# Optimization experiments

Measured on AMD Instinct MI355X. Metric: run time of the kernel, lower is better.

The kernel has to match this reference:

```python
import jax, jax.numpy as jnp
import numpy as np

B, D, E, T, P = 65536, 256, 256, 128, 8  # batch, memory_dim, edge_feat_dim, time_dim, num_prototypes
LN_EPS = 1e-6
NORM_EPS = 1e-6


def _layer_norm(x, w, b):
    mu = jnp.mean(x, axis=-1, keepdims=True)
    var = jnp.mean(jnp.square(x - mu), axis=-1, keepdims=True)
    return (x - mu) / jnp.sqrt(var + LN_EPS) * w + b


def setup_inputs() -> dict:
    key = jax.random.key(0)
    ks = jax.random.split(key, 10)
    qin = D + E + T            # query_proj in_features
    gin = 2 * D + T            # gate_proj in_features
    return {
        "raw_memory": jax.random.normal(ks[0], (B, D), dtype=jnp.float32),
        "node_features": jax.random.normal(ks[1], (B, D), dtype=jnp.float32),
        "edge_features": jax.random.normal(ks[2], (B, E), dtype=jnp.float32),
        "time_encoding": jax.random.normal(ks[3], (B, T), dtype=jnp.float32),
        "prototypes": jax.random.normal(ks[4], (B, P, D), dtype=jnp.float32),
        # learned params (xavier gain=0.1 -> small)
        "Wq": jax.random.normal(ks[5], (D, qin), dtype=jnp.float32) * (0.1 * np.sqrt(2.0 / (D + qin))),
        "bq": jnp.zeros((D,), dtype=jnp.float32),
        "Wg": jax.random.normal(ks[6], (1, gin), dtype=jnp.float32) * (0.1 * np.sqrt(2.0 / (1 + gin))),
        "bg": jnp.zeros((1,), dtype=jnp.float32),
        "temperature": jnp.ones((1,), dtype=jnp.float32),
        "ln_w": jnp.ones((D,), dtype=jnp.float32),
        "ln_b": jnp.zeros((D,), dtype=jnp.float32),
    }


def reference(raw_memory, node_features, edge_features, time_encoding, prototypes,
              Wq, bq, Wg, bg, temperature, ln_w, ln_b):
    # query projection (inputs are finite so _sanitize_tensor is identity)
    q_in = jnp.concatenate([raw_memory, edge_features, time_encoding], axis=-1)  # [B, D+E+T]
    query = jnp.tanh(_layer_norm(q_in @ Wq.T + bq, ln_w, ln_b))                   # [B, D]

    # cosine similarity to per-node prototypes (F.normalize uses max(norm, eps))
    qn = query / jnp.maximum(jnp.linalg.norm(query, axis=-1, keepdims=True), NORM_EPS)
    pn = prototypes / jnp.maximum(jnp.linalg.norm(prototypes, axis=-1, keepdims=True), NORM_EPS)
    sim = jnp.clip(jnp.einsum('bd,bpd->bp', qn, pn), -10.0, 10.0)                 # [B, P]
    temp = jnp.clip(temperature, 0.5, 5.0)
    sim = sim / (temp + 0.01)

    attn = jnp.clip(jax.nn.softmax(sim, axis=-1), 0.0, 1.0)                       # [B, P]
    candidate = jnp.clip(jnp.einsum('bp,bpd->bd', attn, prototypes), -5.0, 5.0)   # [B, D]

    # gated update
    g_in = jnp.clip(jnp.concatenate([raw_memory, candidate, time_encoding], axis=-1), -50.0, 50.0)
    gate = jax.nn.sigmoid(jnp.clip(g_in @ Wg.T + bg, -10.0, 10.0))                # [B, 1]
    updated = (1.0 - gate) * raw_memory + gate * candidate
    updated = jnp.clip(_layer_norm(updated, ln_w, ln_b), -10.0, 10.0)
    return updated
```

## Files before the change

kernel.cpp:

```cpp
#include <hip/hip_runtime.h>
#include <cstdint>
#include <cstddef>

#define D 256
#define E 256
#define T 128
#define QIN 640
#define P 8
#define R 16
#define KP 648
#define DP 260

typedef __attribute__((ext_vector_type(8))) short bf16x8;
typedef __attribute__((ext_vector_type(4))) float f32x4;

__device__ __forceinline__ ushort f2bf(float f) {
  uint32_t u = __float_as_uint(f);
  u += 0x7fffu + ((u >> 16) & 1u);
  return (ushort)(u >> 16);
}

__device__ __forceinline__ float wsum(float v) {
#pragma unroll
  for (int o = 32; o > 0; o >>= 1) v += __shfl_xor(v, o, 64);
  return v;
}

__device__ __forceinline__ void wsum2(float& a, float& b) {
#pragma unroll
  for (int o = 32; o > 0; o >>= 1) {
    a += __shfl_xor(a, o, 64);
    b += __shfl_xor(b, o, 64);
  }
}

__device__ __forceinline__ float clampf(float x, float lo, float hi) {
  return fminf(fmaxf(x, lo), hi);
}

__global__ void prep_w2_kernel(const float* __restrict__ Wq, ushort* __restrict__ W2) {
  const int idx = blockIdx.x * 256 + threadIdx.x;
  const int n = idx / QIN;
  const int k = idx - n * QIN;
  W2[((((k >> 3) * D + n) << 3)) + (k & 7)] = f2bf(Wq[idx]);
}

template <bool PRE>
__global__ __launch_bounds__(256, 4) void fused_kernel(
    const float* __restrict__ raw, const float* __restrict__ edge,
    const float* __restrict__ tim, const float* __restrict__ proto,
    const float* __restrict__ Wq, const ushort* __restrict__ W2,
    const float* __restrict__ bq, const float* __restrict__ Wg,
    const float* __restrict__ bg, const float* __restrict__ temp,
    const float* __restrict__ lnw, const float* __restrict__ lnb,
    float* __restrict__ out) {
  __shared__ ushort qa[R][KP];
  __shared__ float qpre[R][DP];

  const int tid = threadIdx.x;
  const int r0 = blockIdx.x * R;

#pragma unroll
  for (int it = 0; it < (R * QIN / 4) / 256; ++it) {
    const int flat = it * 256 + tid;
    const int r = flat / (QIN / 4);
    const int p4 = (flat - r * (QIN / 4)) * 4;
    const size_t g = (size_t)(r0 + r);
    float4 v;
    if (p4 < D)          v = *(const float4*)(raw + g * D + p4);
    else if (p4 < D + E) v = *(const float4*)(edge + g * E + (p4 - D));
    else                 v = *(const float4*)(tim + g * T + (p4 - D - E));
    ushort4 h;
    h.x = f2bf(v.x); h.y = f2bf(v.y); h.z = f2bf(v.z); h.w = f2bf(v.w);
    *(ushort4*)&qa[r][p4] = h;
  }
  __syncthreads();

  const int w = tid >> 6;
  const int lane = tid & 63;
  const int lr = lane & 15;
  const int lh = lane >> 4;

  {
    f32x4 acc[4];
#pragma unroll
    for (int c = 0; c < 4; ++c) acc[c] = (f32x4){0.f, 0.f, 0.f, 0.f};

    for (int kb = 0; kb < QIN; kb += 32) {
      const bf16x8 af = *(const bf16x8*)&qa[lr][kb + lh * 8];
#pragma unroll
      for (int c = 0; c < 4; ++c) {
        const int n = w * 64 + c * 16 + lr;
        bf16x8 bfv;
        if (PRE) {
          bfv = *(const bf16x8*)&W2[(((kb >> 3) + lh) * D + n) << 3];
        } else {
          const float* src = Wq + (size_t)n * QIN + kb + lh * 8;
          const float4 a0 = *(const float4*)src;
          const float4 a1 = *(const float4*)(src + 4);
          bfv[0] = (short)f2bf(a0.x); bfv[1] = (short)f2bf(a0.y);
          bfv[2] = (short)f2bf(a0.z); bfv[3] = (short)f2bf(a0.w);
          bfv[4] = (short)f2bf(a1.x); bfv[5] = (short)f2bf(a1.y);
          bfv[6] = (short)f2bf(a1.z); bfv[7] = (short)f2bf(a1.w);
        }
        acc[c] = __builtin_amdgcn_mfma_f32_16x16x32_bf16(af, bfv, acc[c], 0, 0, 0);
      }
    }

#pragma unroll
    for (int c = 0; c < 4; ++c) {
      const int n = w * 64 + c * 16 + lr;
      const float bqv = bq[n];
#pragma unroll
      for (int i = 0; i < 4; ++i) qpre[lh * 4 + i][n] = acc[c][i] + bqv;
    }
  }
  __syncthreads();

  const float4 lnw4 = *(const float4*)(lnw + 4 * lane);
  const float4 lnb4 = *(const float4*)(lnb + 4 * lane);
  const float lw[4] = {lnw4.x, lnw4.y, lnw4.z, lnw4.w};
  const float lb[4] = {lnb4.x, lnb4.y, lnb4.z, lnb4.w};
  const float4 wga = *(const float4*)(Wg + 4 * lane);
  const float4 wgb = *(const float4*)(Wg + D + 4 * lane);
  const float2 wgt = *(const float2*)(Wg + 2 * D + 2 * lane);
  const float bgv = bg[0];
  const float invt = 1.0f / (clampf(temp[0], 0.5f, 5.0f) + 0.01f);

  for (int r = w; r < R; r += 4) {
    const size_t g = (size_t)(r0 + r);

    const float4 x4 = *(const float4*)&qpre[r][4 * lane];
    float x[4] = {x4.x, x4.y, x4.z, x4.w};
    float s = x[0] + x[1] + x[2] + x[3];
    const float mu = wsum(s) * (1.0f / 256.0f);
    float dx[4];
    float v = 0.f;
#pragma unroll
    for (int i = 0; i < 4; ++i) { dx[i] = x[i] - mu; v += dx[i] * dx[i]; }
    const float rstd = 1.0f / sqrtf(wsum(v) * (1.0f / 256.0f) + 1e-6f);
    float q[4];
    float qs = 0.f;
#pragma unroll
    for (int i = 0; i < 4; ++i) {
      q[i] = tanhf(dx[i] * rstd * lw[i] + lb[i]);
      qs += q[i] * q[i];
    }
    const float qdiv = fmaxf(sqrtf(wsum(qs)), 1e-6f);

    const float* pb = proto + (g * P) * D + 4 * lane;
    float pv[P][4];
    float sim[P];
#pragma unroll
    for (int p = 0; p < P; ++p) {
      const float4 p4 = *(const float4*)(pb + (size_t)p * D);
      pv[p][0] = p4.x; pv[p][1] = p4.y; pv[p][2] = p4.z; pv[p][3] = p4.w;
      float dt = q[0] * p4.x + q[1] * p4.y + q[2] * p4.z + q[3] * p4.w;
      float pn = p4.x * p4.x + p4.y * p4.y + p4.z * p4.z + p4.w * p4.w;
      wsum2(dt, pn);
      const float pdiv = fmaxf(sqrtf(pn), 1e-6f);
      sim[p] = clampf(dt / (qdiv * pdiv), -10.0f, 10.0f) * invt;
    }

    float m = sim[0];
#pragma unroll
    for (int p = 1; p < P; ++p) m = fmaxf(m, sim[p]);
    float es[P];
    float ssum = 0.f;
#pragma unroll
    for (int p = 0; p < P; ++p) { es[p] = expf(sim[p] - m); ssum += es[p]; }
    const float sinv = 1.0f / ssum;
    float cand[4] = {0.f, 0.f, 0.f, 0.f};
#pragma unroll
    for (int p = 0; p < P; ++p) {
      const float a = clampf(es[p] * sinv, 0.0f, 1.0f);
#pragma unroll
      for (int i = 0; i < 4; ++i) cand[i] = fmaf(a, pv[p][i], cand[i]);
    }
#pragma unroll
    for (int i = 0; i < 4; ++i) cand[i] = clampf(cand[i], -5.0f, 5.0f);

    const float4 raw4 = *(const float4*)(raw + g * D + 4 * lane);
    const float rr[4] = {raw4.x, raw4.y, raw4.z, raw4.w};
    const float2 t2 = *(const float2*)(tim + g * T + 2 * lane);
    float gsum =
        clampf(rr[0], -50.f, 50.f) * wga.x + clampf(rr[1], -50.f, 50.f) * wga.y +
        clampf(rr[2], -50.f, 50.f) * wga.z + clampf(rr[3], -50.f, 50.f) * wga.w +
        clampf(cand[0], -50.f, 50.f) * wgb.x + clampf(cand[1], -50.f, 50.f) * wgb.y +
        clampf(cand[2], -50.f, 50.f) * wgb.z + clampf(cand[3], -50.f, 50.f) * wgb.w +
        clampf(t2.x, -50.f, 50.f) * wgt.x + clampf(t2.y, -50.f, 50.f) * wgt.y;
    const float z = clampf(wsum(gsum) + bgv, -10.0f, 10.0f);
    const float gate = 1.0f / (1.0f + expf(-z));

    float upd[4];
    float s2 = 0.f;
#pragma unroll
    for (int i = 0; i < 4; ++i) {
      upd[i] = (1.0f - gate) * rr[i] + gate * cand[i];
      s2 += upd[i];
    }
    const float mu2 = wsum(s2) * (1.0f / 256.0f);
    float du[4];
    float v2 = 0.f;
#pragma unroll
    for (int i = 0; i < 4; ++i) { du[i] = upd[i] - mu2; v2 += du[i] * du[i]; }
    const float rstd2 = 1.0f / sqrtf(wsum(v2) * (1.0f / 256.0f) + 1e-6f);
    float4 y;
    y.x = clampf(du[0] * rstd2 * lw[0] + lb[0], -10.0f, 10.0f);
    y.y = clampf(du[1] * rstd2 * lw[1] + lb[1], -10.0f, 10.0f);
    y.z = clampf(du[2] * rstd2 * lw[2] + lb[2], -10.0f, 10.0f);
    y.w = clampf(du[3] * rstd2 * lw[3] + lb[3], -10.0f, 10.0f);
    *(float4*)(out + g * D + 4 * lane) = y;
  }
}

extern "C" void kernel_launch(void* const* d_in, const int* in_sizes, int n_in,
                              void* d_out, int out_size, void* d_ws, size_t ws_size,
                              hipStream_t stream) {
  const float* raw   = (const float*)d_in[0];
  const float* edge  = (const float*)d_in[2];
  const float* tim   = (const float*)d_in[3];
  const float* proto = (const float*)d_in[4];
  const float* Wq    = (const float*)d_in[5];
  const float* bq    = (const float*)d_in[6];
  const float* Wg    = (const float*)d_in[7];
  const float* bg    = (const float*)d_in[8];
  const float* temp  = (const float*)d_in[9];
  const float* lnw   = (const float*)d_in[10];
  const float* lnb   = (const float*)d_in[11];
  float* out = (float*)d_out;

  const int B = in_sizes[0] / D;
  const int nblk = B / R;

  const bool pre = ws_size >= (size_t)(QIN * D * sizeof(ushort));
  if (pre) {
    ushort* W2 = (ushort*)d_ws;
    prep_w2_kernel<<<(QIN * D) / 256, 256, 0, stream>>>(Wq, W2);
    fused_kernel<true><<<nblk, 256, 0, stream>>>(raw, edge, tim, proto, Wq, W2,
                                                 bq, Wg, bg, temp, lnw, lnb, out);
  } else {
    fused_kernel<false><<<nblk, 256, 0, stream>>>(raw, edge, tim, proto, Wq,
                                                  (const ushort*)nullptr, bq, Wg,
                                                  bg, temp, lnw, lnb, out);
  }
}
```

Before: 227.1 us.

## Prefetch prototype rows into registers before GEMM and double-buffer across rows

Issues the first row's prototype loads for each wave before the MFMA projection loop, so their latency hides behind the GEMM. The per-row epilogue is unrolled into four calls that software-pipeline the next row's prototype loads (and hoist raw/time loads) while the current row is computed. This adds about 64 extra live VGPRs per thread under a launch bound of 4 blocks per CU, which risks spills or lower occupancy.

```diff
diff --git a/kernel.cpp b/kernel.cpp
--- a/kernel.cpp
+++ b/kernel.cpp
@@ -80,6 +80,13 @@
   const int lane = tid & 63;
   const int lr = lane & 15;
   const int lh = lane >> 4;
+
+  float4 bufA[P], bufB[P];
+  {
+    const float* pb0 = proto + ((size_t)(r0 + w) * P) * D + 4 * lane;
+#pragma unroll
+    for (int p = 0; p < P; ++p) bufA[p] = *(const float4*)(pb0 + (size_t)p * D);
+  }
 
   {
     f32x4 acc[4];
@@ -127,8 +134,16 @@
   const float bgv = bg[0];
   const float invt = 1.0f / (clampf(temp[0], 0.5f, 5.0f) + 0.01f);
 
-  for (int r = w; r < R; r += 4) {
+  auto process = [&](int r, float4* cur, float4* nxt, bool pre) {
     const size_t g = (size_t)(r0 + r);
+
+    if (pre) {
+      const float* pbn = proto + ((g + 4) * P) * D + 4 * lane;
+#pragma unroll
+      for (int p = 0; p < P; ++p) nxt[p] = *(const float4*)(pbn + (size_t)p * D);
+    }
+    const float4 raw4 = *(const float4*)(raw + g * D + 4 * lane);
+    const float2 t2 = *(const float2*)(tim + g * T + 2 * lane);
 
     const float4 x4 = *(const float4*)&qpre[r][4 * lane];
     float x[4] = {x4.x, x4.y, x4.z, x4.w};
@@ -148,13 +163,10 @@
     }
     const float qdiv = fmaxf(sqrtf(wsum(qs)), 1e-6f);
 
-    const float* pb = proto + (g * P) * D + 4 * lane;
-    float pv[P][4];
     float sim[P];
 #pragma unroll
     for (int p = 0; p < P; ++p) {
-      const float4 p4 = *(const float4*)(pb + (size_t)p * D);
-      pv[p][0] = p4.x; pv[p][1] = p4.y; pv[p][2] = p4.z; pv[p][3] = p4.w;
+      const float4 p4 = cur[p];
       float dt = q[0] * p4.x + q[1] * p4.y + q[2] * p4.z + q[3] * p4.w;
       float pn = p4.x * p4.x + p4.y * p4.y + p4.z * p4.z + p4.w * p4.w;
       wsum2(dt, pn);
@@ -165,24 +177,23 @@
     float m = sim[0];
 #pragma unroll
     for (int p = 1; p < P; ++p) m = fmaxf(m, sim[p]);
-    float es[P];
     float ssum = 0.f;
 #pragma unroll
-    for (int p = 0; p < P; ++p) { es[p] = expf(sim[p] - m); ssum += es[p]; }
+    for (int p = 0; p < P; ++p) { sim[p] = expf(sim[p] - m); ssum += sim[p]; }
     const float sinv = 1.0f / ssum;
     float cand[4] = {0.f, 0.f, 0.f, 0.f};
 #pragma unroll
     for (int p = 0; p < P; ++p) {
-      const float a = clampf(es[p] * sinv, 0.0f, 1.0f);
-#pragma unroll
-      for (int i = 0; i < 4; ++i) cand[i] = fmaf(a, pv[p][i], cand[i]);
+      const float a = clampf(sim[p] * sinv, 0.0f, 1.0f);
+      cand[0] = fmaf(a, cur[p].x, cand[0]);
+      cand[1] = fmaf(a, cur[p].y, cand[1]);
+      cand[2] = fmaf(a, cur[p].z, cand[2]);
+      cand[3] = fmaf(a, cur[p].w, cand[3]);
     }
 #pragma unroll
     for (int i = 0; i < 4; ++i) cand[i] = clampf(cand[i], -5.0f, 5.0f);
 
-    const float4 raw4 = *(const float4*)(raw + g * D + 4 * lane);
     const float rr[4] = {raw4.x, raw4.y, raw4.z, raw4.w};
-    const float2 t2 = *(const float2*)(tim + g * T + 2 * lane);
     float gsum =
         clampf(rr[0], -50.f, 50.f) * wga.x + clampf(rr[1], -50.f, 50.f) * wga.y +
         clampf(rr[2], -50.f, 50.f) * wga.z + clampf(rr[3], -50.f, 50.f) * wga.w +
@@ -211,7 +222,12 @@
     y.z = clampf(du[2] * rstd2 * lw[2] + lb[2], -10.0f, 10.0f);
     y.w = clampf(du[3] * rstd2 * lw[3] + lb[3], -10.0f, 10.0f);
     *(float4*)(out + g * D + 4 * lane) = y;
-  }
+  };
+
+  process(w,      bufA, bufB, true);
+  process(w + 4,  bufB, bufA, true);
+  process(w + 8,  bufA, bufB, true);
+  process(w + 12, bufB, bufA, false);
 }
 
 extern "C" void kernel_launch(void* const* d_in, const int* in_sizes, int n_in,
```

Result: faster. 220.2 us (-3.0%).

## Split fused kernel into query-projection and prototype-streaming kernels via bf16 workspace

Applied to the files above, without the earlier changes.

Splits the fused kernel into two. One does the GEMM, layer norm and tanh, writing a normalized bf16 query to workspace. The other is a lightweight one-row-per-wave kernel that streams the prototypes and computes the attention, gate and final layer norm. This decouples the bandwidth-heavy prototype reads from the MFMA/LDS phase so the streaming kernel can run at higher occupancy. The cost is extra global traffic for the qn round trip and re-reading raw and time, plus one more launch and bf16 rounding of the normalized query.

```diff
diff --git a/kernel.cpp b/kernel.cpp
--- a/kernel.cpp
+++ b/kernel.cpp
@@ -19,6 +19,9 @@
   u += 0x7fffu + ((u >> 16) & 1u);
   return (ushort)(u >> 16);
 }
+__device__ __forceinline__ float bf2f(ushort h) {
+  return __uint_as_float(((uint32_t)h) << 16);
+}
 
 __device__ __forceinline__ float wsum(float v) {
 #pragma unroll
@@ -45,15 +48,11 @@
   W2[((((k >> 3) * D + n) << 3)) + (k & 7)] = f2bf(Wq[idx]);
 }
 
-template <bool PRE>
-__global__ __launch_bounds__(256, 4) void fused_kernel(
+__global__ __launch_bounds__(256, 4) void qn_kernel(
     const float* __restrict__ raw, const float* __restrict__ edge,
-    const float* __restrict__ tim, const float* __restrict__ proto,
-    const float* __restrict__ Wq, const ushort* __restrict__ W2,
-    const float* __restrict__ bq, const float* __restrict__ Wg,
-    const float* __restrict__ bg, const float* __restrict__ temp,
-    const float* __restrict__ lnw, const float* __restrict__ lnb,
-    float* __restrict__ out) {
+    const float* __restrict__ tim, const ushort* __restrict__ W2,
+    const float* __restrict__ bq, const float* __restrict__ lnw,
+    const float* __restrict__ lnb, ushort* __restrict__ qn) {
   __shared__ ushort qa[R][KP];
   __shared__ float qpre[R][DP];
 
@@ -91,22 +90,194 @@
 #pragma unroll
       for (int c = 0; c < 4; ++c) {
         const int n = w * 64 + c * 16 + lr;
-        bf16x8 bfv;
-        if (PRE) {
-          bfv = *(const bf16x8*)&W2[(((kb >> 3) + lh) * D + n) << 3];
-        } else {
-          const float* src = Wq + (size_t)n * QIN + kb + lh * 8;
-          const float4 a0 = *(const float4*)src;
-          const float4 a1 = *(const float4*)(src + 4);
-          bfv[0] = (short)f2bf(a0.x); bfv[1] = (short)f2bf(a0.y);
-          bfv[2] = (short)f2bf(a0.z); bfv[3] = (short)f2bf(a0.w);
-          bfv[4] = (short)f2bf(a1.x); bfv[5] = (short)f2bf(a1.y);
-          bfv[6] = (short)f2bf(a1.z); bfv[7] = (short)f2bf(a1.w);
-        }
+        const bf16x8 bfv = *(const bf16x8*)&W2[(((kb >> 3) + lh) * D + n) << 3];
         acc[c] = __builtin_amdgcn_mfma_f32_16x16x32_bf16(af, bfv, acc[c], 0, 0, 0);
       }
     }
-
+#pragma unroll
+    for (int c = 0; c < 4; ++c) {
+      const int n = w * 64 + c * 16 + lr;
+      const float bqv = bq[n];
+#pragma unroll
+      for (int i = 0; i < 4; ++i) qpre[lh * 4 + i][n] = acc[c][i] + bqv;
+    }
+  }
+  __syncthreads();
+
+  const float4 lnw4 = *(const float4*)(lnw + 4 * lane);
+  const float4 lnb4 = *(const float4*)(lnb + 4 * lane);
+  const float lw[4] = {lnw4.x, lnw4.y, lnw4.z, lnw4.w};
+  const float lb[4] = {lnb4.x, lnb4.y, lnb4.z, lnb4.w};
+
+  for (int r = w; r < R; r += 4) {
+    const size_t g = (size_t)(r0 + r);
+    const float4 x4 = *(const float4*)&qpre[r][4 * lane];
+    float x[4] = {x4.x, x4.y, x4.z, x4.w};
+    const float mu = wsum(x[0] + x[1] + x[2] + x[3]) * (1.0f / 256.0f);
+    float dx[4];
+    float v = 0.f;
+#pragma unroll
+    for (int i = 0; i < 4; ++i) { dx[i] = x[i] - mu; v += dx[i] * dx[i]; }
+    const float rstd = 1.0f / sqrtf(wsum(v) * (1.0f / 256.0f) + 1e-6f);
+    float q[4];
+    float qs = 0.f;
+#pragma unroll
+    for (int i = 0; i < 4; ++i) {
+      q[i] = tanhf(dx[i] * rstd * lw[i] + lb[i]);
+      qs += q[i] * q[i];
+    }
+    const float qinv = 1.0f / fmaxf(sqrtf(wsum(qs)), 1e-6f);
+    ushort4 h;
+    h.x = f2bf(q[0] * qinv); h.y = f2bf(q[1] * qinv);
+    h.z = f2bf(q[2] * qinv); h.w = f2bf(q[3] * qinv);
+    *(ushort4*)(qn + g * D + 4 * lane) = h;
+  }
+}
+
+__global__ __launch_bounds__(256, 5) void stream_kernel(
+    const float* __restrict__ raw, const float* __restrict__ tim,
+    const float* __restrict__ proto, const ushort* __restrict__ qn,
+    const float* __restrict__ Wg, const float* __restrict__ bg,
+    const float* __restrict__ temp, const float* __restrict__ lnw,
+    const float* __restrict__ lnb, float* __restrict__ out) {
+  const int tid = threadIdx.x;
+  const int w = tid >> 6;
+  const int lane = tid & 63;
+  const size_t g = (size_t)blockIdx.x * 4 + w;
+
+  const float* pb = proto + (g * P) * D + 4 * lane;
+  float4 pv[P];
+#pragma unroll
+  for (int p = 0; p < P; ++p) pv[p] = *(const float4*)(pb + (size_t)p * D);
+  const ushort4 qh = *(const ushort4*)(qn + g * D + 4 * lane);
+  const float4 raw4 = *(const float4*)(raw + g * D + 4 * lane);
+  const float2 t2 = *(const float2*)(tim + g * T + 2 * lane);
+
+  const float4 lnw4 = *(const float4*)(lnw + 4 * lane);
+  const float4 lnb4 = *(const float4*)(lnb + 4 * lane);
+  const float4 wga = *(const float4*)(Wg + 4 * lane);
+  const float4 wgb = *(const float4*)(Wg + D + 4 * lane);
+  const float2 wgt = *(const float2*)(Wg + 2 * D + 2 * lane);
+  const float bgv = bg[0];
+  const float invt = 1.0f / (clampf(temp[0], 0.5f, 5.0f) + 0.01f);
+
+  const float q[4] = {bf2f(qh.x), bf2f(qh.y), bf2f(qh.z), bf2f(qh.w)};
+
+  float sim[P];
+#pragma unroll
+  for (int p = 0; p < P; ++p) {
+    const float4 p4 = pv[p];
+    float dt = q[0] * p4.x + q[1] * p4.y + q[2] * p4.z + q[3] * p4.w;
+    float pn = p4.x * p4.x + p4.y * p4.y + p4.z * p4.z + p4.w * p4.w;
+    wsum2(dt, pn);
+    const float pdiv = fmaxf(sqrtf(pn), 1e-6f);
+    sim[p] = clampf(dt / pdiv, -10.0f, 10.0f) * invt;
+  }
+
+  float m = sim[0];
+#pragma unroll
+  for (int p = 1; p < P; ++p) m = fmaxf(m, sim[p]);
+  float ssum = 0.f;
+#pragma unroll
+  for (int p = 0; p < P; ++p) { sim[p] = expf(sim[p] - m); ssum += sim[p]; }
+  const float sinv = 1.0f / ssum;
+  float cand[4] = {0.f, 0.f, 0.f, 0.f};
+#pragma unroll
+  for (int p = 0; p < P; ++p) {
+    const float a = clampf(sim[p] * sinv, 0.0f, 1.0f);
+    cand[0] = fmaf(a, pv[p].x, cand[0]);
+    cand[1] = fmaf(a, pv[p].y, cand[1]);
+    cand[2] = fmaf(a, pv[p].z, cand[2]);
+    cand[3] = fmaf(a, pv[p].w, cand[3]);
+  }
+#pragma unroll
+  for (int i = 0; i < 4; ++i) cand[i] = clampf(cand[i], -5.0f, 5.0f);
+
+  const float rr[4] = {raw4.x, raw4.y, raw4.z, raw4.w};
+  float gsum =
+      clampf(rr[0], -50.f, 50.f) * wga.x + clampf(rr[1], -50.f, 50.f) * wga.y +
+      clampf(rr[2], -50.f, 50.f) * wga.z + clampf(rr[3], -50.f, 50.f) * wga.w +
+      clampf(cand[0], -50.f, 50.f) * wgb.x + clampf(cand[1], -50.f, 50.f) * wgb.y +
+      clampf(cand[2], -50.f, 50.f) * wgb.z + clampf(cand[3], -50.f, 50.f) * wgb.w +
+      clampf(t2.x, -50.f, 50.f) * wgt.x + clampf(t2.y, -50.f, 50.f) * wgt.y;
+  const float z = clampf(wsum(gsum) + bgv, -10.0f, 10.0f);
+  const float gate = 1.0f / (1.0f + expf(-z));
+
+  float upd[4];
+  float s2 = 0.f;
+#pragma unroll
+  for (int i = 0; i < 4; ++i) {
+    upd[i] = (1.0f - gate) * rr[i] + gate * cand[i];
+    s2 += upd[i];
+  }
+  const float mu2 = wsum(s2) * (1.0f / 256.0f);
+  float du[4];
+  float v2 = 0.f;
+#pragma unroll
+  for (int i = 0; i < 4; ++i) { du[i] = upd[i] - mu2; v2 += du[i] * du[i]; }
+  const float rstd2 = 1.0f / sqrtf(wsum(v2) * (1.0f / 256.0f) + 1e-6f);
+  float4 y;
+  y.x = clampf(du[0] * rstd2 * lnw4.x + lnb4.x, -10.0f, 10.0f);
+  y.y = clampf(du[1] * rstd2 * lnw4.y + lnb4.y, -10.0f, 10.0f);
+  y.z = clampf(du[2] * rstd2 * lnw4.z + lnb4.z, -10.0f, 10.0f);
+  y.w = clampf(du[3] * rstd2 * lnw4.w + lnb4.w, -10.0f, 10.0f);
+  *(float4*)(out + g * D + 4 * lane) = y;
+}
+
+__global__ __launch_bounds__(256, 4) void fused_kernel(
+    const float* __restrict__ raw, const float* __restrict__ edge,
+    const float* __restrict__ tim, const float* __restrict__ proto,
+    const float* __restrict__ Wq, const float* __restrict__ bq,
+    const float* __restrict__ Wg, const float* __restrict__ bg,
+    const float* __restrict__ temp, const float* __restrict__ lnw,
+    const float* __restrict__ lnb, float* __restrict__ out) {
+  __shared__ ushort qa[R][KP];
+  __shared__ float qpre[R][DP];
+
+  const int tid = threadIdx.x;
+  const int r0 = blockIdx.x * R;
+
+#pragma unroll
+  for (int it = 0; it < (R * QIN / 4) / 256; ++it) {
+    const int flat = it * 256 + tid;
+    const int r = flat / (QIN / 4);
+    const int p4 = (flat - r * (QIN / 4)) * 4;
+    const size_t g = (size_t)(r0 + r);
+    float4 v;
+    if (p4 < D)          v = *(const float4*)(raw + g * D + p4);
+    else if (p4 < D + E) v = *(const float4*)(edge + g * E + (p4 - D));
+    else                 v = *(const float4*)(tim + g * T + (p4 - D - E));
+    ushort4 h;
+    h.x = f2bf(v.x); h.y = f2bf(v.y); h.z = f2bf(v.z); h.w = f2bf(v.w);
+    *(ushort4*)&qa[r][p4] = h;
+  }
+  __syncthreads();
+
+  const int w = tid >> 6;
+  const int lane = tid & 63;
+  const int lr = lane & 15;
+  const int lh = lane >> 4;
+
+  {
+    f32x4 acc[4];
+#pragma unroll
+    for (int c = 0; c < 4; ++c) acc[c] = (f32x4){0.f, 0.f, 0.f, 0.f};
+    for (int kb = 0; kb < QIN; kb += 32) {
+      const bf16x8 af = *(const bf16x8*)&qa[lr][kb + lh * 8];
+#pragma unroll
+      for (int c = 0; c < 4; ++c) {
+        const int n = w * 64 + c * 16 + lr;
+        const float* src = Wq + (size_t)n * QIN + kb + lh * 8;
+        const float4 a0 = *(const float4*)src;
+        const float4 a1 = *(const float4*)(src + 4);
+        bf16x8 bfv;
+        bfv[0] = (short)f2bf(a0.x); bfv[1] = (short)f2bf(a0.y);
+        bfv[2] = (short)f2bf(a0.z); bfv[3] = (short)f2bf(a0.w);
+        bfv[4] = (short)f2bf(a1.x); bfv[5] = (short)f2bf(a1.y);
+        bfv[6] = (short)f2bf(a1.z); bfv[7] = (short)f2bf(a1.w);
+        acc[c] = __builtin_amdgcn_mfma_f32_16x16x32_bf16(af, bfv, acc[c], 0, 0, 0);
+      }
+    }
 #pragma unroll
     for (int c = 0; c < 4; ++c) {
       const int n = w * 64 + c * 16 + lr;
@@ -129,11 +300,9 @@
 
   for (int r = w; r < R; r += 4) {
     const size_t g = (size_t)(r0 + r);
-
     const float4 x4 = *(const float4*)&qpre[r][4 * lane];
     float x[4] = {x4.x, x4.y, x4.z, x4.w};
-    float s = x[0] + x[1] + x[2] + x[3];
-    const float mu = wsum(s) * (1.0f / 256.0f);
+    const float mu = wsum(x[0] + x[1] + x[2] + x[3]) * (1.0f / 256.0f);
     float dx[4];
     float v = 0.f;
 #pragma unroll
@@ -161,19 +330,17 @@
       const float pdiv = fmaxf(sqrtf(pn), 1e-6f);
       sim[p] = clampf(dt / (qdiv * pdiv), -10.0f, 10.0f) * invt;
     }
-
     float m = sim[0];
 #pragma unroll
     for (int p = 1; p < P; ++p) m = fmaxf(m, sim[p]);
-    float es[P];
     float ssum = 0.f;
 #pragma unroll
-    for (int p = 0; p < P; ++p) { es[p] = expf(sim[p] - m); ssum += es[p]; }
+    for (int p = 0; p < P; ++p) { sim[p] = expf(sim[p] - m); ssum += sim[p]; }
     const float sinv = 1.0f / ssum;
     float cand[4] = {0.f, 0.f, 0.f, 0.f};
 #pragma unroll
     for (int p = 0; p < P; ++p) {
-      const float a = clampf(es[p] * sinv, 0.0f, 1.0f);
+      const float a = clampf(sim[p] * sinv, 0.0f, 1.0f);
 #pragma unroll
       for (int i = 0; i < 4; ++i) cand[i] = fmaf(a, pv[p][i], cand[i]);
     }
@@ -231,17 +398,18 @@
   float* out = (float*)d_out;
 
   const int B = in_sizes[0] / D;
-  const int nblk = B / R;
-
-  const bool pre = ws_size >= (size_t)(QIN * D * sizeof(ushort));
-  if (pre) {
+
+  const size_t w2_bytes = (size_t)QIN * D * sizeof(ushort);
+  const size_t qn_bytes = (size_t)B * D * sizeof(ushort);
+  if (ws_size >= w2_bytes + qn_bytes) {
     ushort* W2 = (ushort*)d_ws;
+    ushort* qn = (ushort*)((char*)d_ws + w2_bytes);
     prep_w2_kernel<<<(QIN * D) / 256, 256, 0, stream>>>(Wq, W2);
-    fused_kernel<true><<<nblk, 256, 0, stream>>>(raw, edge, tim, proto, Wq, W2,
-                                                 bq, Wg, bg, temp, lnw, lnb, out);
+    qn_kernel<<<B / R, 256, 0, stream>>>(raw, edge, tim, W2, bq, lnw, lnb, qn);
+    stream_kernel<<<B / 4, 256, 0, stream>>>(raw, tim, proto, qn, Wg, bg, temp,
+                                             lnw, lnb, out);
   } else {
-    fused_kernel<false><<<nblk, 256, 0, stream>>>(raw, edge, tim, proto, Wq,
-                                                  (const ushort*)nullptr, bq, Wg,
-                                                  bg, temp, lnw, lnb, out);
-  }
-}
+    fused_kernel<<<B / R, 256, 0, stream>>>(raw, edge, tim, proto, Wq, bq, Wg,
+                                            bg, temp, lnw, lnb, out);
+  }
+}
```

After: 248.9 us. 9.6% more time.

## Double rows per block, load MFMA A operands directly, half-wave rows in epilogue

Applied to the files above, without the earlier changes.

Each block now handles 32 rows instead of 16, so every bf16 weight fragment feeds two MFMA tiles and global weight traffic per row is halved. The LDS staging of the concatenated input is dropped; A fragments are loaded and converted to bf16 straight from global memory. The per-row epilogue now gives each half-wave its own row, using 32-lane reductions, and batches prototype loads and shuffle reductions across all 8 prototypes for more memory-level parallelism. In exchange it uses more registers and re-reads the first four prototype rows for the candidate sum, and the A loads are strided, less coalesced global reads.

```diff
diff --git a/kernel.cpp b/kernel.cpp
--- a/kernel.cpp
+++ b/kernel.cpp
@@ -7,8 +7,7 @@
 #define T 128
 #define QIN 640
 #define P 8
-#define R 16
-#define KP 648
+#define R 32
 #define DP 260
 
 typedef __attribute__((ext_vector_type(8))) short bf16x8;
@@ -20,18 +19,21 @@
   return (ushort)(u >> 16);
 }
 
-__device__ __forceinline__ float wsum(float v) {
-#pragma unroll
-  for (int o = 32; o > 0; o >>= 1) v += __shfl_xor(v, o, 64);
+__device__ __forceinline__ bf16x8 cvt8(const float* p) {
+  const float4 a = *(const float4*)p;
+  const float4 b = *(const float4*)(p + 4);
+  bf16x8 r;
+  r[0] = (short)f2bf(a.x); r[1] = (short)f2bf(a.y);
+  r[2] = (short)f2bf(a.z); r[3] = (short)f2bf(a.w);
+  r[4] = (short)f2bf(b.x); r[5] = (short)f2bf(b.y);
+  r[6] = (short)f2bf(b.z); r[7] = (short)f2bf(b.w);
+  return r;
+}
+
+__device__ __forceinline__ float wsum32(float v) {
+#pragma unroll
+  for (int o = 16; o > 0; o >>= 1) v += __shfl_xor(v, o, 64);
   return v;
-}
-
-__device__ __forceinline__ void wsum2(float& a, float& b) {
-#pragma unroll
-  for (int o = 32; o > 0; o >>= 1) {
-    a += __shfl_xor(a, o, 64);
-    b += __shfl_xor(b, o, 64);
-  }
 }
 
 __device__ __forceinline__ float clampf(float x, float lo, float hi) {
@@ -54,163 +56,222 @@
     const float* __restrict__ bg, const float* __restrict__ temp,
     const float* __restrict__ lnw, const float* __restrict__ lnb,
     float* __restrict__ out) {
-  __shared__ ushort qa[R][KP];
   __shared__ float qpre[R][DP];
 
   const int tid = threadIdx.x;
   const int r0 = blockIdx.x * R;
-
-#pragma unroll
-  for (int it = 0; it < (R * QIN / 4) / 256; ++it) {
-    const int flat = it * 256 + tid;
-    const int r = flat / (QIN / 4);
-    const int p4 = (flat - r * (QIN / 4)) * 4;
-    const size_t g = (size_t)(r0 + r);
-    float4 v;
-    if (p4 < D)          v = *(const float4*)(raw + g * D + p4);
-    else if (p4 < D + E) v = *(const float4*)(edge + g * E + (p4 - D));
-    else                 v = *(const float4*)(tim + g * T + (p4 - D - E));
-    ushort4 h;
-    h.x = f2bf(v.x); h.y = f2bf(v.y); h.z = f2bf(v.z); h.w = f2bf(v.w);
-    *(ushort4*)&qa[r][p4] = h;
-  }
-  __syncthreads();
-
   const int w = tid >> 6;
   const int lane = tid & 63;
   const int lr = lane & 15;
   const int lh = lane >> 4;
 
   {
-    f32x4 acc[4];
-#pragma unroll
-    for (int c = 0; c < 4; ++c) acc[c] = (f32x4){0.f, 0.f, 0.f, 0.f};
-
+    f32x4 acc0[4], acc1[4];
+#pragma unroll
+    for (int c = 0; c < 4; ++c) {
+      acc0[c] = (f32x4){0.f, 0.f, 0.f, 0.f};
+      acc1[c] = (f32x4){0.f, 0.f, 0.f, 0.f};
+    }
+    const size_t gA0 = (size_t)(r0 + lr);
+    const size_t gA1 = (size_t)(r0 + 16 + lr);
+
+#pragma unroll
     for (int kb = 0; kb < QIN; kb += 32) {
-      const bf16x8 af = *(const bf16x8*)&qa[lr][kb + lh * 8];
+      const float* s0;
+      const float* s1;
+      int o;
+      if (kb < D)            { s0 = raw  + gA0 * D; s1 = raw  + gA1 * D; o = kb; }
+      else if (kb < D + E)   { s0 = edge + gA0 * E; s1 = edge + gA1 * E; o = kb - D; }
+      else                   { s0 = tim  + gA0 * T; s1 = tim  + gA1 * T; o = kb - D - E; }
+      o += lh * 8;
+      const bf16x8 a0 = cvt8(s0 + o);
+      const bf16x8 a1 = cvt8(s1 + o);
 #pragma unroll
       for (int c = 0; c < 4; ++c) {
         const int n = w * 64 + c * 16 + lr;
-        bf16x8 bfv;
+        bf16x8 bv;
         if (PRE) {
-          bfv = *(const bf16x8*)&W2[(((kb >> 3) + lh) * D + n) << 3];
+          bv = *(const bf16x8*)&W2[(((kb >> 3) + lh) * D + n) << 3];
         } else {
-          const float* src = Wq + (size_t)n * QIN + kb + lh * 8;
-          const float4 a0 = *(const float4*)src;
-          const float4 a1 = *(const float4*)(src + 4);
-          bfv[0] = (short)f2bf(a0.x); bfv[1] = (short)f2bf(a0.y);
-          bfv[2] = (short)f2bf(a0.z); bfv[3] = (short)f2bf(a0.w);
-          bfv[4] = (short)f2bf(a1.x); bfv[5] = (short)f2bf(a1.y);
-          bfv[6] = (short)f2bf(a1.z); bfv[7] = (short)f2bf(a1.w);
+          bv = cvt8(Wq + (size_t)n * QIN + kb + lh * 8);
         }
-        acc[c] = __builtin_amdgcn_mfma_f32_16x16x32_bf16(af, bfv, acc[c], 0, 0, 0);
-      }
-    }
-
+        acc0[c] = __builtin_amdgcn_mfma_f32_16x16x32_bf16(a0, bv, acc0[c], 0, 0, 0);
+        acc1[c] = __builtin_amdgcn_mfma_f32_16x16x32_bf16(a1, bv, acc1[c], 0, 0, 0);
+      }
+    }
 #pragma unroll
     for (int c = 0; c < 4; ++c) {
       const int n = w * 64 + c * 16 + lr;
       const float bqv = bq[n];
 #pragma unroll
-      for (int i = 0; i < 4; ++i) qpre[lh * 4 + i][n] = acc[c][i] + bqv;
+      for (int i = 0; i < 4; ++i) {
+        qpre[lh * 4 + i][n]      = acc0[c][i] + bqv;
+        qpre[16 + lh * 4 + i][n] = acc1[c][i] + bqv;
+      }
     }
   }
   __syncthreads();
 
-  const float4 lnw4 = *(const float4*)(lnw + 4 * lane);
-  const float4 lnb4 = *(const float4*)(lnb + 4 * lane);
-  const float lw[4] = {lnw4.x, lnw4.y, lnw4.z, lnw4.w};
-  const float lb[4] = {lnb4.x, lnb4.y, lnb4.z, lnb4.w};
-  const float4 wga = *(const float4*)(Wg + 4 * lane);
-  const float4 wgb = *(const float4*)(Wg + D + 4 * lane);
-  const float2 wgt = *(const float2*)(Wg + 2 * D + 2 * lane);
+  const int h = lane >> 5;
+  const int l32 = lane & 31;
+  const int d0 = l32 * 4;
+  const int d1 = 128 + l32 * 4;
+
+  const float4 lw0 = *(const float4*)(lnw + d0);
+  const float4 lw1 = *(const float4*)(lnw + d1);
+  const float4 lb0 = *(const float4*)(lnb + d0);
+  const float4 lb1 = *(const float4*)(lnb + d1);
+  const float4 wr0 = *(const float4*)(Wg + d0);
+  const float4 wr1 = *(const float4*)(Wg + d1);
+  const float4 wc0 = *(const float4*)(Wg + D + d0);
+  const float4 wc1 = *(const float4*)(Wg + D + d1);
+  const float4 wt  = *(const float4*)(Wg + 2 * D + l32 * 4);
   const float bgv = bg[0];
   const float invt = 1.0f / (clampf(temp[0], 0.5f, 5.0f) + 0.01f);
 
-  for (int r = w; r < R; r += 4) {
+#pragma unroll 1
+  for (int j = 0; j < 4; ++j) {
+    const int r = j * 8 + w * 2 + h;
     const size_t g = (size_t)(r0 + r);
-
-    const float4 x4 = *(const float4*)&qpre[r][4 * lane];
-    float x[4] = {x4.x, x4.y, x4.z, x4.w};
-    float s = x[0] + x[1] + x[2] + x[3];
-    const float mu = wsum(s) * (1.0f / 256.0f);
-    float dx[4];
+    const float* pb = proto + g * (size_t)(P * D);
+
+    const float4 ra0 = *(const float4*)(raw + g * D + d0);
+    const float4 ra1 = *(const float4*)(raw + g * D + d1);
+    const float4 t4  = *(const float4*)(tim + g * T + l32 * 4);
+
+    const float4 x0 = *(const float4*)&qpre[r][d0];
+    const float4 x1 = *(const float4*)&qpre[r][d1];
+    float x[8] = {x0.x, x0.y, x0.z, x0.w, x1.x, x1.y, x1.z, x1.w};
+    float s = 0.f;
+#pragma unroll
+    for (int i = 0; i < 8; ++i) s += x[i];
+    const float mu = wsum32(s) * (1.0f / 256.0f);
     float v = 0.f;
 #pragma unroll
-    for (int i = 0; i < 4; ++i) { dx[i] = x[i] - mu; v += dx[i] * dx[i]; }
-    const float rstd = 1.0f / sqrtf(wsum(v) * (1.0f / 256.0f) + 1e-6f);
-    float q[4];
+    for (int i = 0; i < 8; ++i) { x[i] -= mu; v += x[i] * x[i]; }
+    const float rstd = 1.0f / sqrtf(wsum32(v) * (1.0f / 256.0f) + 1e-6f);
+    const float lwv[8] = {lw0.x, lw0.y, lw0.z, lw0.w, lw1.x, lw1.y, lw1.z, lw1.w};
+    const float lbv[8] = {lb0.x, lb0.y, lb0.z, lb0.w, lb1.x, lb1.y, lb1.z, lb1.w};
+    float q[8];
     float qs = 0.f;
 #pragma unroll
-    for (int i = 0; i < 4; ++i) {
-      q[i] = tanhf(dx[i] * rstd * lw[i] + lb[i]);
+    for (int i = 0; i < 8; ++i) {
+      q[i] = tanhf(x[i] * rstd * lwv[i] + lbv[i]);
       qs += q[i] * q[i];
     }
-    const float qdiv = fmaxf(sqrtf(wsum(qs)), 1e-6f);
-
-    const float* pb = proto + (g * P) * D + 4 * lane;
-    float pv[P][4];
+    const float qdiv = fmaxf(sqrtf(wsum32(qs)), 1e-6f);
+
+    float dt[8], pn[8];
+#pragma unroll
+    for (int cch = 0; cch < 2; ++cch) {
+      float4 A0[4], A1[4];
+#pragma unroll
+      for (int p = 0; p < 4; ++p) {
+        A0[p] = *(const float4*)(pb + (size_t)(cch * 4 + p) * D + d0);
+        A1[p] = *(const float4*)(pb + (size_t)(cch * 4 + p) * D + d1);
+      }
+#pragma unroll
+      for (int p = 0; p < 4; ++p) {
+        const int pi = cch * 4 + p;
+        dt[pi] = q[0] * A0[p].x + q[1] * A0[p].y + q[2] * A0[p].z + q[3] * A0[p].w +
+                 q[4] * A1[p].x + q[5] * A1[p].y + q[6] * A1[p].z + q[7] * A1[p].w;
+        pn[pi] = A0[p].x * A0[p].x + A0[p].y * A0[p].y + A0[p].z * A0[p].z +
+                 A0[p].w * A0[p].w + A1[p].x * A1[p].x + A1[p].y * A1[p].y +
+                 A1[p].z * A1[p].z + A1[p].w * A1[p].w;
+      }
+    }
+#pragma unroll
+    for (int o = 16; o > 0; o >>= 1) {
+#pragma unroll
+      for (int p = 0; p < P; ++p) {
+        dt[p] += __shfl_xor(dt[p], o, 64);
+        pn[p] += __shfl_xor(pn[p], o, 64);
+      }
+    }
+
+    float4 C0[4], C1[4];
+#pragma unroll
+    for (int p = 0; p < 4; ++p) {
+      C0[p] = *(const float4*)(pb + (size_t)p * D + d0);
+      C1[p] = *(const float4*)(pb + (size_t)p * D + d1);
+    }
+
     float sim[P];
 #pragma unroll
     for (int p = 0; p < P; ++p) {
-      const float4 p4 = *(const float4*)(pb + (size_t)p * D);
-      pv[p][0] = p4.x; pv[p][1] = p4.y; pv[p][2] = p4.z; pv[p][3] = p4.w;
-      float dt = q[0] * p4.x + q[1] * p4.y + q[2] * p4.z + q[3] * p4.w;
-      float pn = p4.x * p4.x + p4.y * p4.y + p4.z * p4.z + p4.w * p4.w;
-      wsum2(dt, pn);
-      const float pdiv = fmaxf(sqrtf(pn), 1e-6f);
-      sim[p] = clampf(dt / (qdiv * pdiv), -10.0f, 10.0f) * invt;
-    }
-
+      const float pdiv = fmaxf(sqrtf(pn[p]), 1e-6f);
+      sim[p] = clampf(dt[p] / (qdiv * pdiv), -10.0f, 10.0f) * invt;
+    }
     float m = sim[0];
 #pragma unroll
     for (int p = 1; p < P; ++p) m = fmaxf(m, sim[p]);
-    float es[P];
     float ssum = 0.f;
 #pragma unroll
-    for (int p = 0; p < P; ++p) { es[p] = expf(sim[p] - m); ssum += es[p]; }
+    for (int p = 0; p < P; ++p) { sim[p] = expf(sim[p] - m); ssum += sim[p]; }
     const float sinv = 1.0f / ssum;
-    float cand[4] = {0.f, 0.f, 0.f, 0.f};
-#pragma unroll
-    for (int p = 0; p < P; ++p) {
-      const float a = clampf(es[p] * sinv, 0.0f, 1.0f);
-#pragma unroll
-      for (int i = 0; i < 4; ++i) cand[i] = fmaf(a, pv[p][i], cand[i]);
-    }
-#pragma unroll
-    for (int i = 0; i < 4; ++i) cand[i] = clampf(cand[i], -5.0f, 5.0f);
-
-    const float4 raw4 = *(const float4*)(raw + g * D + 4 * lane);
-    const float rr[4] = {raw4.x, raw4.y, raw4.z, raw4.w};
-    const float2 t2 = *(const float2*)(tim + g * T + 2 * lane);
-    float gsum =
-        clampf(rr[0], -50.f, 50.f) * wga.x + clampf(rr[1], -50.f, 50.f) * wga.y +
-        clampf(rr[2], -50.f, 50.f) * wga.z + clampf(rr[3], -50.f, 50.f) * wga.w +
-        clampf(cand[0], -50.f, 50.f) * wgb.x + clampf(cand[1], -50.f, 50.f) * wgb.y +
-        clampf(cand[2], -50.f, 50.f) * wgb.z + clampf(cand[3], -50.f, 50.f) * wgb.w +
-        clampf(t2.x, -50.f, 50.f) * wgt.x + clampf(t2.y, -50.f, 50.f) * wgt.y;
-    const float z = clampf(wsum(gsum) + bgv, -10.0f, 10.0f);
+#pragma unroll
+    for (int p = 0; p < P; ++p) sim[p] = clampf(sim[p] * sinv, 0.0f, 1.0f);
+
+    float cd[8] = {0.f, 0.f, 0.f, 0.f, 0.f, 0.f, 0.f, 0.f};
+#pragma unroll
+    for (int p = 0; p < 4; ++p) {
+      cd[0] = fmaf(sim[p], C0[p].x, cd[0]); cd[1] = fmaf(sim[p], C0[p].y, cd[1]);
+      cd[2] = fmaf(sim[p], C0[p].z, cd[2]); cd[3] = fmaf(sim[p], C0[p].w, cd[3]);
+      cd[4] = fmaf(sim[p], C1[p].x, cd[4]); cd[5] = fmaf(sim[p], C1[p].y, cd[5]);
+      cd[6] = fmaf(sim[p], C1[p].z, cd[6]); cd[7] = fmaf(sim[p], C1[p].w, cd[7]);
+    }
+#pragma unroll
+    for (int p = 0; p < 4; ++p) {
+      C0[p] = *(const float4*)(pb + (size_t)(4 + p) * D + d0);
+      C1[p] = *(const float4*)(pb + (size_t)(4 + p) * D + d1);
+    }
+#pragma unroll
+    for (int p = 0; p < 4; ++p) {
+      const float a = sim[4 + p];
+      cd[0] = fmaf(a, C0[p].x, cd[0]); cd[1] = fmaf(a, C0[p].y, cd[1]);
+      cd[2] = fmaf(a, C0[p].z, cd[2]); cd[3] = fmaf(a, C0[p].w, cd[3]);
+      cd[4] = fmaf(a, C1[p].x, cd[4]); cd[5] = fmaf(a, C1[p].y, cd[5]);
+      cd[6] = fmaf(a, C1[p].z, cd[6]); cd[7] = fmaf(a, C1[p].w, cd[7]);
+    }
+#pragma unroll
+    for (int i = 0; i < 8; ++i) cd[i] = clampf(cd[i], -5.0f, 5.0f);
+
+    const float rr[8] = {ra0.x, ra0.y, ra0.z, ra0.w, ra1.x, ra1.y, ra1.z, ra1.w};
+    const float wrv[8] = {wr0.x, wr0.y, wr0.z, wr0.w, wr1.x, wr1.y, wr1.z, wr1.w};
+    const float wcv[8] = {wc0.x, wc0.y, wc0.z, wc0.w, wc1.x, wc1.y, wc1.z, wc1.w};
+    float gsum = clampf(t4.x, -50.f, 50.f) * wt.x + clampf(t4.y, -50.f, 50.f) * wt.y +
+                 clampf(t4.z, -50.f, 50.f) * wt.z + clampf(t4.w, -50.f, 50.f) * wt.w;
+#pragma unroll
+    for (int i = 0; i < 8; ++i) {
+      gsum += clampf(rr[i], -50.f, 50.f) * wrv[i];
+      gsum += clampf(cd[i], -50.f, 50.f) * wcv[i];
+    }
+    const float z = clampf(wsum32(gsum) + bgv, -10.0f, 10.0f);
     const float gate = 1.0f / (1.0f + expf(-z));
 
-    float upd[4];
+    float upd[8];
     float s2 = 0.f;
 #pragma unroll
-    for (int i = 0; i < 4; ++i) {
-      upd[i] = (1.0f - gate) * rr[i] + gate * cand[i];
+    for (int i = 0; i < 8; ++i) {
+      upd[i] = (1.0f - gate) * rr[i] + gate * cd[i];
       s2 += upd[i];
     }
-    const float mu2 = wsum(s2) * (1.0f / 256.0f);
-    float du[4];
+    const float mu2 = wsum32(s2) * (1.0f / 256.0f);
     float v2 = 0.f;
 #pragma unroll
-    for (int i = 0; i < 4; ++i) { du[i] = upd[i] - mu2; v2 += du[i] * du[i]; }
-    const float rstd2 = 1.0f / sqrtf(wsum(v2) * (1.0f / 256.0f) + 1e-6f);
-    float4 y;
-    y.x = clampf(du[0] * rstd2 * lw[0] + lb[0], -10.0f, 10.0f);
-    y.y = clampf(du[1] * rstd2 * lw[1] + lb[1], -10.0f, 10.0f);
-    y.z = clampf(du[2] * rstd2 * lw[2] + lb[2], -10.0f, 10.0f);
-    y.w = clampf(du[3] * rstd2 * lw[3] + lb[3], -10.0f, 10.0f);
-    *(float4*)(out + g * D + 4 * lane) = y;
+    for (int i = 0; i < 8; ++i) { upd[i] -= mu2; v2 += upd[i] * upd[i]; }
+    const float rstd2 = 1.0f / sqrtf(wsum32(v2) * (1.0f / 256.0f) + 1e-6f);
+    float4 y0, y1;
+    y0.x = clampf(upd[0] * rstd2 * lwv[0] + lbv[0], -10.0f, 10.0f);
+    y0.y = clampf(upd[1] * rstd2 * lwv[1] + lbv[1], -10.0f, 10.0f);
+    y0.z = clampf(upd[2] * rstd2 * lwv[2] + lbv[2], -10.0f, 10.0f);
+    y0.w = clampf(upd[3] * rstd2 * lwv[3] + lbv[3], -10.0f, 10.0f);
+    y1.x = clampf(upd[4] * rstd2 * lwv[4] + lbv[4], -10.0f, 10.0f);
+    y1.y = clampf(upd[5] * rstd2 * lwv[5] + lbv[5], -10.0f, 10.0f);
+    y1.z = clampf(upd[6] * rstd2 * lwv[6] + lbv[6], -10.0f, 10.0f);
+    y1.w = clampf(upd[7] * rstd2 * lwv[7] + lbv[7], -10.0f, 10.0f);
+    *(float4*)(out + g * D + d0) = y0;
+    *(float4*)(out + g * D + d1) = y1;
   }
 }
 
@@ -233,8 +294,7 @@
   const int B = in_sizes[0] / D;
   const int nblk = B / R;
 
-  const bool pre = ws_size >= (size_t)(QIN * D * sizeof(ushort));
-  if (pre) {
+  if (ws_size >= (size_t)QIN * D * sizeof(ushort)) {
     ushort* W2 = (ushort*)d_ws;
     prep_w2_kernel<<<(QIN * D) / 256, 256, 0, stream>>>(Wq, W2);
     fused_kernel<true><<<nblk, 256, 0, stream>>>(raw, edge, tim, proto, Wq, W2,
```

Measured after the change: 266.1 us. 1.17x slower.
